# Optimization experiments

Measured on AMD Instinct MI355X. Metric: run time of the kernel, lower is better.

## Reference

```python
import jax, jax.numpy as jnp
import numpy as np

B, S, D_IN, D_OUT, R = 4, 1024, 1024, 1024, 8

def setup_inputs() -> dict:
    key = jax.random.key(0)
    k1, k2, k3, k4, k5 = jax.random.split(key, 5)
    scale = 1.0 / np.sqrt(D_IN)
    return {
        "x": jax.random.normal(k1, (B, S, D_IN), dtype=jnp.float32),
        "A_params": jax.random.normal(k2, (B, S, D_OUT, R), dtype=jnp.float32) * 0.02,
        "B_params": jax.random.normal(k3, (B, S, R, D_IN), dtype=jnp.float32) * 0.02,
        "W": jax.random.normal(k4, (D_OUT, D_IN), dtype=jnp.float32) * scale,
        "b": jax.random.normal(k5, (D_OUT,), dtype=jnp.float32) * scale,
    }

def reference(x, A_params, B_params, W, b):
    # base linear: y = x @ W^T + b  -> [B, S, D_OUT]
    base_out = jnp.einsum('bsi,oi->bso', x, W) + b
    # per-token low-rank update: (x @ B^T) @ A^T
    inter = jnp.einsum('bsi,bsri->bsr', x, B_params)           # [B, S, R]
    adaptation = jnp.einsum('bsr,bsor->bso', inter, A_params)  # [B, S, D_OUT]
    return base_out + adaptation
```

## Files before the change

### kernel.cpp

```cpp
#include <hip/hip_runtime.h>
#include <hip/hip_bf16.h>
#include <stdint.h>

#define TOKENS 4096
#define DIN 1024
#define DOUT 1024
#define RANK 8
#define BM 128
#define BN 64
#define BK 64

typedef __attribute__((ext_vector_type(4))) float f32x4;
typedef __attribute__((ext_vector_type(8))) short short8;

__device__ __forceinline__ unsigned short f2bf(float f) {
    union { float f; unsigned u; } v; v.f = f;
    unsigned r = v.u + 0x7FFFu + ((v.u >> 16) & 1u);
    return (unsigned short)(r >> 16);
}

__global__ __launch_bounds__(256) void k_convert_w(const float* __restrict__ W,
                                                   ushort* __restrict__ Wb) {
    int i = blockIdx.x * 256 + threadIdx.x;
    float4 v = ((const float4*)W)[i];
    ushort4 u;
    u.x = f2bf(v.x); u.y = f2bf(v.y); u.z = f2bf(v.z); u.w = f2bf(v.w);
    ((ushort4*)Wb)[i] = u;
}

__global__ __launch_bounds__(256) void k_inter(const float* __restrict__ x,
                                               const float* __restrict__ Bp,
                                               float* __restrict__ inter,
                                               ushort* __restrict__ xb) {
    const int t = blockIdx.x;
    const int tid = threadIdx.x;
    const int lane = tid & 63, wave = tid >> 6;

    float4 xv = ((const float4*)(x + (size_t)t * DIN))[tid];

    ushort4 u;
    u.x = f2bf(xv.x); u.y = f2bf(xv.y); u.z = f2bf(xv.z); u.w = f2bf(xv.w);
    ((ushort4*)(xb + (size_t)t * DIN))[tid] = u;

    const float4* B4 = (const float4*)(Bp + (size_t)t * RANK * DIN);
    float acc[RANK];
#pragma unroll
    for (int r = 0; r < RANK; ++r) {
        float4 bv = B4[r * 256 + tid];
        acc[r] = xv.x * bv.x + xv.y * bv.y + xv.z * bv.z + xv.w * bv.w;
    }

    __shared__ float part[4][RANK];
#pragma unroll
    for (int r = 0; r < RANK; ++r) {
        float v = acc[r];
#pragma unroll
        for (int off = 32; off > 0; off >>= 1) v += __shfl_xor(v, off, 64);
        if (lane == 0) part[wave][r] = v;
    }
    __syncthreads();
    if (tid < RANK)
        inter[(size_t)t * RANK + tid] =
            part[0][tid] + part[1][tid] + part[2][tid] + part[3][tid];
}

__global__ __launch_bounds__(256) void k_gemm_fused(const ushort* __restrict__ Xb,
                                                    const ushort* __restrict__ Wb,
                                                    const float* __restrict__ bias,
                                                    const float* __restrict__ inter,
                                                    const float* __restrict__ Ap,
                                                    float* __restrict__ out) {
    __shared__ ushort As[2][BM * BK];
    __shared__ ushort Bs[2][BN * BK];
    __shared__ float sInter[BM * 8];
    __shared__ float sBias[BN];

    const int tid = threadIdx.x;
    const int lane = tid & 63, wave = tid >> 6;
    const int wm = wave >> 1, wn = wave & 1;

    const int bid = blockIdx.x;
    const int swz = (bid & 7) * 64 + (bid >> 3);
    const int M0 = (swz >> 4) * BM;
    const int N0 = (swz & 15) * BN;

    const int col16 = lane & 15;
    const int kg = lane >> 4;

    ((float4*)sInter)[tid] = ((const float4*)(inter + (size_t)M0 * RANK))[tid];
    if (tid < 16) ((float4*)sBias)[tid] = ((const float4*)(bias + N0))[tid];

    const float* Abase = Ap + ((size_t)(M0 + wm * 64 + kg * 4) * DOUT +
                               (N0 + wn * 32 + col16)) * RANK;

    auto stage = [&](int b, int kt) {
#pragma unroll
        for (int st = 0; st < 4; ++st) {
            int flat = st * 256 + tid;
            int row = flat >> 3, ch = flat & 7;
            const ushort* g = Xb + (size_t)(M0 + row) * DIN + kt + ch * 8;
            __builtin_amdgcn_global_load_lds(
                (const __attribute__((address_space(1))) void*)g,
                (__attribute__((address_space(3))) void*)(&As[b][flat * 8]), 16, 0, 0);
        }
#pragma unroll
        for (int st = 0; st < 2; ++st) {
            int flat = st * 256 + tid;
            int row = flat >> 3, ch = flat & 7;
            const ushort* g = Wb + (size_t)(N0 + row) * DIN + kt + ch * 8;
            __builtin_amdgcn_global_load_lds(
                (const __attribute__((address_space(1))) void*)g,
                (__attribute__((address_space(3))) void*)(&Bs[b][flat * 8]), 16, 0, 0);
        }
    };

    stage(0, 0);
    asm volatile("s_waitcnt vmcnt(0) lgkmcnt(0)" ::: "memory");
    __builtin_amdgcn_s_barrier();

    f32x4 acc[4][2] = {};

#pragma unroll
    for (int it = 0; it < 16; ++it) {
        const int cur = it & 1;
        if (it < 15) stage(cur ^ 1, (it + 1) * BK);

        const int nf = it >> 3, mf = (it >> 1) & 3, rg0 = (it & 1) * 2;
        const float* Ae0 = Abase + ((size_t)(mf * 16 + rg0) * DOUT + nf * 16) * RANK;
        const float* Ae1 = Ae0 + (size_t)DOUT * RANK;
        float4 a00 = ((const float4*)Ae0)[0];
        float4 a01 = ((const float4*)Ae0)[1];
        float4 a10 = ((const float4*)Ae1)[0];
        float4 a11 = ((const float4*)Ae1)[1];

#pragma unroll
        for (int ks = 0; ks < 2; ++ks) {
            short8 a[4], b[2];
#pragma unroll
            for (int m4 = 0; m4 < 4; ++m4)
                a[m4] = *(const short8*)(&As[cur][(wm * 64 + m4 * 16 + col16) * BK + ks * 32 + kg * 8]);
#pragma unroll
            for (int n2 = 0; n2 < 2; ++n2)
                b[n2] = *(const short8*)(&Bs[cur][(wn * 32 + n2 * 16 + col16) * BK + ks * 32 + kg * 8]);
#pragma unroll
            for (int m4 = 0; m4 < 4; ++m4)
#pragma unroll
                for (int n2 = 0; n2 < 2; ++n2)
                    acc[m4][n2] = __builtin_amdgcn_mfma_f32_16x16x32_bf16(
                        a[m4], b[n2], acc[m4][n2], 0, 0, 0);
        }

        const int mloc0 = wm * 64 + mf * 16 + kg * 4 + rg0;
        const float4* iv0 = (const float4*)(sInter + mloc0 * 8);
        const float4* iv1 = (const float4*)(sInter + (mloc0 + 1) * 8);
        float4 i00 = iv0[0], i01 = iv0[1], i10 = iv1[0], i11 = iv1[1];
        float d0 = a00.x * i00.x + a00.y * i00.y + a00.z * i00.z + a00.w * i00.w +
                   a01.x * i01.x + a01.y * i01.y + a01.z * i01.z + a01.w * i01.w;
        float d1 = a10.x * i10.x + a10.y * i10.y + a10.z * i10.z + a10.w * i10.w +
                   a11.x * i11.x + a11.y * i11.y + a11.z * i11.z + a11.w * i11.w;
        acc[mf][nf][rg0] += d0;
        acc[mf][nf][rg0 + 1] += d1;

        asm volatile("s_waitcnt vmcnt(0)" ::: "memory");
        __builtin_amdgcn_s_barrier();
    }

#pragma unroll
    for (int nf = 0; nf < 2; ++nf) {
        const int oc = wn * 32 + nf * 16 + col16;
        const int o = N0 + oc;
        const float bb = sBias[oc];
#pragma unroll
        for (int mf = 0; mf < 4; ++mf) {
#pragma unroll
            for (int rg = 0; rg < 4; ++rg) {
                const int m = M0 + wm * 64 + mf * 16 + kg * 4 + rg;
                out[(size_t)m * DOUT + o] = acc[mf][nf][rg] + bb;
            }
        }
    }
}

extern "C" void kernel_launch(void* const* d_in, const int* in_sizes, int n_in,
                              void* d_out, int out_size, void* d_ws, size_t ws_size,
                              hipStream_t stream) {
    const float* x    = (const float*)d_in[0];
    const float* Ap   = (const float*)d_in[1];
    const float* Bp   = (const float*)d_in[2];
    const float* W    = (const float*)d_in[3];
    const float* bias = (const float*)d_in[4];
    float* out = (float*)d_out;

    ushort* xb = (ushort*)d_ws;
    ushort* Wb = xb + (size_t)TOKENS * DIN;
    float* inter = (float*)(Wb + (size_t)DOUT * DIN);

    hipLaunchKernelGGL(k_convert_w, dim3(DOUT * DIN / 1024), dim3(256), 0, stream, W, Wb);
    hipLaunchKernelGGL(k_inter, dim3(TOKENS), dim3(256), 0, stream, x, Bp, inter, xb);
    hipLaunchKernelGGL(k_gemm_fused, dim3((TOKENS / BM) * (DOUT / BN)), dim3(256), 0, stream,
                       xb, Wb, bias, inter, Ap, out);
}
```

Before: 73.29 us.

## Halve GEMM M-tile and drop LDS double buffering to raise occupancy

```diff
diff --git a/kernel.cpp b/kernel.cpp
--- a/kernel.cpp
+++ b/kernel.cpp
@@ -6,7 +6,7 @@
 #define DIN 1024
 #define DOUT 1024
 #define RANK 8
-#define BM 128
+#define BM 64
 #define BN 64
 #define BK 64
 
@@ -64,14 +64,14 @@
             part[0][tid] + part[1][tid] + part[2][tid] + part[3][tid];
 }
 
-__global__ __launch_bounds__(256) void k_gemm_fused(const ushort* __restrict__ Xb,
-                                                    const ushort* __restrict__ Wb,
-                                                    const float* __restrict__ bias,
-                                                    const float* __restrict__ inter,
-                                                    const float* __restrict__ Ap,
-                                                    float* __restrict__ out) {
-    __shared__ ushort As[2][BM * BK];
-    __shared__ ushort Bs[2][BN * BK];
+__global__ __launch_bounds__(256, 4) void k_gemm_fused(const ushort* __restrict__ Xb,
+                                                       const ushort* __restrict__ Wb,
+                                                       const float* __restrict__ bias,
+                                                       const float* __restrict__ inter,
+                                                       const float* __restrict__ Ap,
+                                                       float* __restrict__ out) {
+    __shared__ ushort As[BM * BK];
+    __shared__ ushort Bs[BN * BK];
     __shared__ float sInter[BM * 8];
     __shared__ float sBias[BN];
 
@@ -80,28 +80,33 @@
     const int wm = wave >> 1, wn = wave & 1;
 
     const int bid = blockIdx.x;
-    const int swz = (bid & 7) * 64 + (bid >> 3);
+    const int swz = (bid & 7) * 128 + (bid >> 3);
     const int M0 = (swz >> 4) * BM;
     const int N0 = (swz & 15) * BN;
 
     const int col16 = lane & 15;
     const int kg = lane >> 4;
 
-    ((float4*)sInter)[tid] = ((const float4*)(inter + (size_t)M0 * RANK))[tid];
+    if (tid < 128) ((float4*)sInter)[tid] = ((const float4*)(inter + (size_t)M0 * RANK))[tid];
     if (tid < 16) ((float4*)sBias)[tid] = ((const float4*)(bias + N0))[tid];
 
-    const float* Abase = Ap + ((size_t)(M0 + wm * 64 + kg * 4) * DOUT +
+    const float* Abase = Ap + ((size_t)(M0 + wm * 32 + kg * 4) * DOUT +
                                (N0 + wn * 32 + col16)) * RANK;
 
-    auto stage = [&](int b, int kt) {
+    f32x4 acc[2][2] = {};
+
 #pragma unroll
-        for (int st = 0; st < 4; ++st) {
+    for (int it = 0; it < 16; ++it) {
+        const int kt = it * BK;
+        __syncthreads();
+#pragma unroll
+        for (int st = 0; st < 2; ++st) {
             int flat = st * 256 + tid;
             int row = flat >> 3, ch = flat & 7;
             const ushort* g = Xb + (size_t)(M0 + row) * DIN + kt + ch * 8;
             __builtin_amdgcn_global_load_lds(
                 (const __attribute__((address_space(1))) void*)g,
-                (__attribute__((address_space(3))) void*)(&As[b][flat * 8]), 16, 0, 0);
+                (__attribute__((address_space(3))) void*)(As + flat * 8), 16, 0, 0);
         }
 #pragma unroll
         for (int st = 0; st < 2; ++st) {
@@ -110,59 +115,38 @@
             const ushort* g = Wb + (size_t)(N0 + row) * DIN + kt + ch * 8;
             __builtin_amdgcn_global_load_lds(
                 (const __attribute__((address_space(1))) void*)g,
-                (__attribute__((address_space(3))) void*)(&Bs[b][flat * 8]), 16, 0, 0);
+                (__attribute__((address_space(3))) void*)(Bs + flat * 8), 16, 0, 0);
         }
-    };
 
-    stage(0, 0);
-    asm volatile("s_waitcnt vmcnt(0) lgkmcnt(0)" ::: "memory");
-    __builtin_amdgcn_s_barrier();
+        const int nf = it >> 3, mf = (it >> 2) & 1, rg = it & 3;
+        const float4* Ae = (const float4*)(Abase + ((size_t)(mf * 16 + rg) * DOUT + nf * 16) * RANK);
+        float4 a0 = Ae[0], a1 = Ae[1];
 
-    f32x4 acc[4][2] = {};
-
-#pragma unroll
-    for (int it = 0; it < 16; ++it) {
-        const int cur = it & 1;
-        if (it < 15) stage(cur ^ 1, (it + 1) * BK);
-
-        const int nf = it >> 3, mf = (it >> 1) & 3, rg0 = (it & 1) * 2;
-        const float* Ae0 = Abase + ((size_t)(mf * 16 + rg0) * DOUT + nf * 16) * RANK;
-        const float* Ae1 = Ae0 + (size_t)DOUT * RANK;
-        float4 a00 = ((const float4*)Ae0)[0];
-        float4 a01 = ((const float4*)Ae0)[1];
-        float4 a10 = ((const float4*)Ae1)[0];
-        float4 a11 = ((const float4*)Ae1)[1];
+        __syncthreads();
 
 #pragma unroll
         for (int ks = 0; ks < 2; ++ks) {
-            short8 a[4], b[2];
+            short8 a[2], b[2];
 #pragma unroll
-            for (int m4 = 0; m4 < 4; ++m4)
-                a[m4] = *(const short8*)(&As[cur][(wm * 64 + m4 * 16 + col16) * BK + ks * 32 + kg * 8]);
+            for (int m2 = 0; m2 < 2; ++m2)
+                a[m2] = *(const short8*)(As + (wm * 32 + m2 * 16 + col16) * BK + ks * 32 + kg * 8);
 #pragma unroll
             for (int n2 = 0; n2 < 2; ++n2)
-                b[n2] = *(const short8*)(&Bs[cur][(wn * 32 + n2 * 16 + col16) * BK + ks * 32 + kg * 8]);
+                b[n2] = *(const short8*)(Bs + (wn * 32 + n2 * 16 + col16) * BK + ks * 32 + kg * 8);
 #pragma unroll
-            for (int m4 = 0; m4 < 4; ++m4)
+            for (int m2 = 0; m2 < 2; ++m2)
 #pragma unroll
                 for (int n2 = 0; n2 < 2; ++n2)
-                    acc[m4][n2] = __builtin_amdgcn_mfma_f32_16x16x32_bf16(
-                        a[m4], b[n2], acc[m4][n2], 0, 0, 0);
+                    acc[m2][n2] = __builtin_amdgcn_mfma_f32_16x16x32_bf16(
+                        a[m2], b[n2], acc[m2][n2], 0, 0, 0);
         }
 
-        const int mloc0 = wm * 64 + mf * 16 + kg * 4 + rg0;
-        const float4* iv0 = (const float4*)(sInter + mloc0 * 8);
-        const float4* iv1 = (const float4*)(sInter + (mloc0 + 1) * 8);
-        float4 i00 = iv0[0], i01 = iv0[1], i10 = iv1[0], i11 = iv1[1];
-        float d0 = a00.x * i00.x + a00.y * i00.y + a00.z * i00.z + a00.w * i00.w +
-                   a01.x * i01.x + a01.y * i01.y + a01.z * i01.z + a01.w * i01.w;
-        float d1 = a10.x * i10.x + a10.y * i10.y + a10.z * i10.z + a10.w * i10.w +
-                   a11.x * i11.x + a11.y * i11.y + a11.z * i11.z + a11.w * i11.w;
-        acc[mf][nf][rg0] += d0;
-        acc[mf][nf][rg0 + 1] += d1;
-
-        asm volatile("s_waitcnt vmcnt(0)" ::: "memory");
-        __builtin_amdgcn_s_barrier();
+        const int mloc = wm * 32 + mf * 16 + kg * 4 + rg;
+        const float4* iv = (const float4*)(sInter + mloc * 8);
+        float4 i0 = iv[0], i1 = iv[1];
+        float d = a0.x * i0.x + a0.y * i0.y + a0.z * i0.z + a0.w * i0.w +
+                  a1.x * i1.x + a1.y * i1.y + a1.z * i1.z + a1.w * i1.w;
+        acc[mf][nf][rg] += d;
     }
 
 #pragma unroll
@@ -171,10 +155,10 @@
         const int o = N0 + oc;
         const float bb = sBias[oc];
 #pragma unroll
-        for (int mf = 0; mf < 4; ++mf) {
+        for (int mf = 0; mf < 2; ++mf) {
 #pragma unroll
             for (int rg = 0; rg < 4; ++rg) {
-                const int m = M0 + wm * 64 + mf * 16 + kg * 4 + rg;
+                const int m = M0 + wm * 32 + mf * 16 + kg * 4 + rg;
                 out[(size_t)m * DOUT + o] = acc[mf][nf][rg] + bb;
             }
         }
```

After: 77.73 us. +6.1%, slower.

## Prefetch LoRA A rows one iteration ahead and use partial vmcnt waits

Applied to the files above, without the earlier changes.

```diff
diff --git a/kernel.cpp b/kernel.cpp
--- a/kernel.cpp
+++ b/kernel.cpp
@@ -64,12 +64,12 @@
             part[0][tid] + part[1][tid] + part[2][tid] + part[3][tid];
 }
 
-__global__ __launch_bounds__(256) void k_gemm_fused(const ushort* __restrict__ Xb,
-                                                    const ushort* __restrict__ Wb,
-                                                    const float* __restrict__ bias,
-                                                    const float* __restrict__ inter,
-                                                    const float* __restrict__ Ap,
-                                                    float* __restrict__ out) {
+__global__ __launch_bounds__(256, 2) void k_gemm_fused(const ushort* __restrict__ Xb,
+                                                       const ushort* __restrict__ Wb,
+                                                       const float* __restrict__ bias,
+                                                       const float* __restrict__ inter,
+                                                       const float* __restrict__ Ap,
+                                                       float* __restrict__ out) {
     __shared__ ushort As[2][BM * BK];
     __shared__ ushort Bs[2][BN * BK];
     __shared__ float sInter[BM * 8];
@@ -114,24 +114,47 @@
         }
     };
 
+    auto aptr = [&](int e) {
+        const int nf = e >> 3, mf = (e >> 1) & 3, rg0 = (e & 1) * 2;
+        return Abase + ((size_t)(mf * 16 + rg0) * DOUT + nf * 16) * RANK;
+    };
+
+    float4 areg[2][4];
+
+    {
+        const float* Ae0 = aptr(0);
+        areg[0][0] = ((const float4*)Ae0)[0];
+        areg[0][1] = ((const float4*)Ae0)[1];
+        areg[0][2] = ((const float4*)(Ae0 + (size_t)DOUT * RANK))[0];
+        areg[0][3] = ((const float4*)(Ae0 + (size_t)DOUT * RANK))[1];
+    }
+    __builtin_amdgcn_sched_barrier(0);
     stage(0, 0);
-    asm volatile("s_waitcnt vmcnt(0) lgkmcnt(0)" ::: "memory");
-    __builtin_amdgcn_s_barrier();
 
     f32x4 acc[4][2] = {};
 
 #pragma unroll
-    for (int it = 0; it < 16; ++it) {
-        const int cur = it & 1;
-        if (it < 15) stage(cur ^ 1, (it + 1) * BK);
-
-        const int nf = it >> 3, mf = (it >> 1) & 3, rg0 = (it & 1) * 2;
-        const float* Ae0 = Abase + ((size_t)(mf * 16 + rg0) * DOUT + nf * 16) * RANK;
-        const float* Ae1 = Ae0 + (size_t)DOUT * RANK;
-        float4 a00 = ((const float4*)Ae0)[0];
-        float4 a01 = ((const float4*)Ae0)[1];
-        float4 a10 = ((const float4*)Ae1)[0];
-        float4 a11 = ((const float4*)Ae1)[1];
+    for (int t = 0; t < 16; ++t) {
+        const int cur = t & 1;
+
+        if (t < 15) {
+            const float* Ae0 = aptr(t + 1);
+            areg[cur ^ 1][0] = ((const float4*)Ae0)[0];
+            areg[cur ^ 1][1] = ((const float4*)Ae0)[1];
+            areg[cur ^ 1][2] = ((const float4*)(Ae0 + (size_t)DOUT * RANK))[0];
+            areg[cur ^ 1][3] = ((const float4*)(Ae0 + (size_t)DOUT * RANK))[1];
+            __builtin_amdgcn_sched_barrier(0);
+            stage(cur ^ 1, (t + 1) * BK);
+        }
+
+        if (t == 0) {
+            asm volatile("s_waitcnt vmcnt(10) lgkmcnt(0)" ::: "memory");
+        } else if (t < 15) {
+            asm volatile("s_waitcnt vmcnt(10)" ::: "memory");
+        } else {
+            asm volatile("s_waitcnt vmcnt(0)" ::: "memory");
+        }
+        __builtin_amdgcn_s_barrier();
 
 #pragma unroll
         for (int ks = 0; ks < 2; ++ks) {
@@ -150,18 +173,22 @@
                         a[m4], b[n2], acc[m4][n2], 0, 0, 0);
         }
 
-        const int mloc0 = wm * 64 + mf * 16 + kg * 4 + rg0;
-        const float4* iv0 = (const float4*)(sInter + mloc0 * 8);
-        const float4* iv1 = (const float4*)(sInter + (mloc0 + 1) * 8);
-        float4 i00 = iv0[0], i01 = iv0[1], i10 = iv1[0], i11 = iv1[1];
-        float d0 = a00.x * i00.x + a00.y * i00.y + a00.z * i00.z + a00.w * i00.w +
-                   a01.x * i01.x + a01.y * i01.y + a01.z * i01.z + a01.w * i01.w;
-        float d1 = a10.x * i10.x + a10.y * i10.y + a10.z * i10.z + a10.w * i10.w +
-                   a11.x * i11.x + a11.y * i11.y + a11.z * i11.z + a11.w * i11.w;
-        acc[mf][nf][rg0] += d0;
-        acc[mf][nf][rg0 + 1] += d1;
-
-        asm volatile("s_waitcnt vmcnt(0)" ::: "memory");
+        {
+            const int nf = t >> 3, mf = (t >> 1) & 3, rg0 = (t & 1) * 2;
+            const int mloc0 = wm * 64 + mf * 16 + kg * 4 + rg0;
+            const float4* iv0 = (const float4*)(sInter + mloc0 * 8);
+            const float4* iv1 = (const float4*)(sInter + (mloc0 + 1) * 8);
+            float4 i00 = iv0[0], i01 = iv0[1], i10 = iv1[0], i11 = iv1[1];
+            float4 a00 = areg[cur][0], a01 = areg[cur][1];
+            float4 a10 = areg[cur][2], a11 = areg[cur][3];
+            float d0 = a00.x * i00.x + a00.y * i00.y + a00.z * i00.z + a00.w * i00.w +
+                       a01.x * i01.x + a01.y * i01.y + a01.z * i01.z + a01.w * i01.w;
+            float d1 = a10.x * i10.x + a10.y * i10.y + a10.z * i10.z + a10.w * i10.w +
+                       a11.x * i11.x + a11.y * i11.y + a11.z * i11.z + a11.w * i11.w;
+            acc[mf][nf][rg0] += d0;
+            acc[mf][nf][rg0 + 1] += d1;
+        }
+
         __builtin_amdgcn_s_barrier();
     }
 
```

Measured after the change: 74.63 us. No clear change (+1.8%).
